# Optimization experiments

Measured on AMD Instinct MI355X. Metric: run time of the kernel, lower is better.

## Reference

```python
import jax, jax.numpy as jnp
import numpy as np

EMBED_DIM = 1024
NUM_HEADS = 16
HEAD_DIM = EMBED_DIM // NUM_HEADS


def setup_inputs() -> dict:
    key = jax.random.key(0)
    k_x, k_qw, k_qb, k_ow, k_ob = jax.random.split(key, 5)
    B, T, C = 2, 2048, EMBED_DIM
    scale = 1.0 / np.sqrt(C)
    return {
        "x": jax.random.normal(k_x, (B, T, C), dtype=jnp.float32),
        "qkv_w": jax.random.normal(k_qw, (C, 3 * C), dtype=jnp.float32) * scale,
        "qkv_b": jax.random.normal(k_qb, (3 * C,), dtype=jnp.float32) * 0.02,
        "out_w": jax.random.normal(k_ow, (C, C), dtype=jnp.float32) * scale,
        "out_b": jax.random.normal(k_ob, (C,), dtype=jnp.float32) * 0.02,
    }


def reference(x, qkv_w, qkv_b, out_w, out_b):
    # x: (B, T, C). Causal masked multi-head self-attention (eval mode: dropout off).
    B, T, C = x.shape
    H, Dh = NUM_HEADS, HEAD_DIM
    qkv = x @ qkv_w + qkv_b                      # (B, T, 3C)
    qkv = qkv.reshape(B, T, 3, H, Dh)
    q = jnp.transpose(qkv[:, :, 0], (0, 2, 1, 3))  # (B, H, T, Dh)
    k = jnp.transpose(qkv[:, :, 1], (0, 2, 1, 3))
    v = jnp.transpose(qkv[:, :, 2], (0, 2, 1, 3))
    scores = jnp.einsum("bhqd,bhkd->bhqk", q, k) / np.sqrt(Dh)
    causal = jnp.tril(jnp.ones((T, T), dtype=bool))
    scores = jnp.where(causal[None, None], scores, -jnp.inf)
    attn = jax.nn.softmax(scores, axis=-1)        # (B, H, T, T)
    out = jnp.einsum("bhqk,bhkd->bhqd", attn, v)  # (B, H, T, Dh)
    out = jnp.transpose(out, (0, 2, 1, 3)).reshape(B, T, C)
    return out @ out_w + out_b
```

## Files before the change

### kernel.cpp

```cpp
#include <hip/hip_runtime.h>


typedef __bf16 bf16;
typedef __attribute__((ext_vector_type(4))) __bf16 bf16x4;
typedef __attribute__((ext_vector_type(8))) __bf16 bf16x8;
typedef __attribute__((ext_vector_type(4))) float f32x4;

#define T_SEQ 2048
#define NHEAD 16
#define QSCALE 0.1803368801111244f

__device__ __forceinline__ void async16(const bf16* g, const bf16* l) {
    __builtin_amdgcn_global_load_lds(
        (const __attribute__((address_space(1))) void*)g,
        (__attribute__((address_space(3))) void*)l, 16, 0, 0);
}


__global__ void cvt_f32_bf16(const float* __restrict__ in, bf16* __restrict__ out, int n) {
    int i = (blockIdx.x * blockDim.x + threadIdx.x) * 4;
    if (i < n) {
        float4 v = *(const float4*)(in + i);
        bf16x4 o;
        o.x = (bf16)v.x; o.y = (bf16)v.y; o.z = (bf16)v.z; o.w = (bf16)v.w;
        *(bf16x4*)(out + i) = o;
    }
}

__global__ void transpose_cvt(const float* __restrict__ in, bf16* __restrict__ out,
                              int K_, int N_) {
    __shared__ float tile[32][33];
    int k0 = blockIdx.x * 32, n0 = blockIdx.y * 32;
    int tx = threadIdx.x, ty = threadIdx.y;
    for (int r = 0; r < 32; r += 8)
        tile[ty + r][tx] = in[(k0 + ty + r) * N_ + n0 + tx];
    __syncthreads();
    for (int r = 0; r < 32; r += 8)
        out[(n0 + ty + r) * K_ + k0 + tx] = (bf16)tile[tx][ty + r];
}


__global__ __launch_bounds__(256) void gemm_qkv(
    const bf16* __restrict__ A, const bf16* __restrict__ Bt,
    const float* __restrict__ bias,
    bf16* __restrict__ Qo, bf16* __restrict__ Ko, bf16* __restrict__ Vt) {
    __shared__ __align__(16) bf16 As[128 * 32];
    __shared__ __align__(16) bf16 Bs[128 * 32];
    const int t = threadIdx.x;
    const int lane = t & 63, wave = t >> 6;
    const int l15 = lane & 15, quad = lane >> 4;
    const int wm = wave & 1, wn = wave >> 1;
    const int m0 = blockIdx.y * 128, n0 = blockIdx.x * 128;

    f32x4 acc[4][4] = {};

    const bf16* ag = A + (m0 + (t >> 2)) * 1024 + (t & 3) * 8;
    const bf16* bg = Bt + (n0 + (t >> 2)) * 1024 + (t & 3) * 8;
    bf16* as0 = As + wave * 512;
    bf16* as1 = As + 2048 + wave * 512;
    bf16* bs0 = Bs + wave * 512;
    bf16* bs1 = Bs + 2048 + wave * 512;

    for (int k0 = 0; k0 < 1024; k0 += 32) {
        async16(ag + k0, as0);
        async16(ag + 64 * 1024 + k0, as1);
        async16(bg + k0, bs0);
        async16(bg + 64 * 1024 + k0, bs1);
        __syncthreads();
        bf16x8 af[4], bfr[4];
        for (int i = 0; i < 4; i++)
            af[i] = *(const bf16x8*)(As + (wm * 64 + i * 16 + l15) * 32 + quad * 8);
        for (int j = 0; j < 4; j++)
            bfr[j] = *(const bf16x8*)(Bs + (wn * 64 + j * 16 + l15) * 32 + quad * 8);
        for (int i = 0; i < 4; i++)
            for (int j = 0; j < 4; j++)
                acc[i][j] = __builtin_amdgcn_mfma_f32_16x16x32_bf16(af[i], bfr[j], acc[i][j], 0, 0, 0);
        __syncthreads();
    }

    for (int i = 0; i < 4; i++) {
        for (int j = 0; j < 4; j++) {
            int col = n0 + wn * 64 + j * 16 + l15;
            float bv = bias[col];
            int sec = col >> 10, c2 = col & 1023, h = c2 >> 6, d = c2 & 63;
            for (int r = 0; r < 4; r++) {
                int row = m0 + wm * 64 + i * 16 + quad * 4 + r;
                int b = row >> 11, tt = row & 2047;
                int bh = b * NHEAD + h;
                float v = acc[i][j][r] + bv;
                if (sec == 0)
                    Qo[(bh * T_SEQ + tt) * 64 + d] = (bf16)(v * QSCALE);
                else if (sec == 1)
                    Ko[(bh * T_SEQ + tt) * 64 + d] = (bf16)v;
                else
                    Vt[(bh * 64 + d) * T_SEQ + tt] = (bf16)v;
            }
        }
    }
}

#define PSTR 64
__global__ __launch_bounds__(256, 4) void attn(
    const bf16* __restrict__ Q, const bf16* __restrict__ K,
    const bf16* __restrict__ Vt, bf16* __restrict__ AO) {
    __shared__ __align__(16) bf16 Ks[2][64 * 64];
    __shared__ __align__(16) bf16 Vs[2][64 * 64];
    __shared__ __align__(16) bf16 Pb[4][16 * PSTR];
    const int lane = threadIdx.x & 63, wave = threadIdx.x >> 6;
    const int l15 = lane & 15, quad = lane >> 4;
    const int lin = blockIdx.x;
    const int s = lin >> 3;
    const int bh = ((lin & 7) << 2) | (s & 3);
    const int k5 = s >> 2;
    const int R = (k5 & 1) ? (k5 >> 1) : (31 - (k5 >> 1));
    const int Rb = R * 64;

    const bf16* qp = Q + (bh * T_SEQ + Rb + wave * 16) * 64;
    const bf16* kp = K + bh * T_SEQ * 64;
    const bf16* vp = Vt + bh * 64 * T_SEQ;
    bf16* pw = &Pb[wave][0];

    bf16x8 qf0 = *(const bf16x8*)(qp + l15 * 64 + quad * 8);
    bf16x8 qf1 = *(const bf16x8*)(qp + l15 * 64 + 32 + quad * 8);

    f32x4 acc[4] = {};
    float lsum[4] = {0.f, 0.f, 0.f, 0.f};

    const int sx = (quad ^ (l15 & 7)) << 3;

    auto stage = [&](int kb, int b) {
        const bf16* kg = kp + kb * 64;
        for (int i = 0; i < 2; i++) {
            int G = (wave * 2 + i) * 64 + lane;
            int key = G >> 3, p = G & 7;
            async16(kg + key * 64 + ((p ^ (key & 7)) << 3), &Ks[b][(wave * 2 + i) * 512]);
        }
        for (int i = 0; i < 2; i++) {
            int d = (wave * 2 + i) * 8 + (lane >> 3);
            async16(vp + d * T_SEQ + kb + (((lane & 7) ^ (d & 7)) << 3),
                    &Vs[b][(wave * 2 + i) * 512]);
        }
    };

    stage(0, 0);
    for (int c = 0; c <= R; c++) {
        __syncthreads();
        if (c < R) stage((c + 1) * 64, (c + 1) & 1);
        const bf16* ksb = &Ks[c & 1][0];
        const bf16* vsb = &Vs[c & 1][0];
        const bool dg = (c == R);
        const int na = dg ? (wave + 1) : 4;
        const int kb = c * 64;

        f32x4 sc[4];
        for (int n = 0; n < 4; n++) {
            if (n < na) {
                const bf16* kbase = ksb + (n * 16 + l15) * 64;
                bf16x8 kf0 = *(const bf16x8*)(kbase + sx);
                bf16x8 kf1 = *(const bf16x8*)(kbase + (sx ^ 32));
                f32x4 z = {};
                z = __builtin_amdgcn_mfma_f32_16x16x32_bf16(qf0, kf0, z, 0, 0, 0);
                z = __builtin_amdgcn_mfma_f32_16x16x32_bf16(qf1, kf1, z, 0, 0, 0);
                sc[n] = z;
            }
        }
        for (int n = 0; n < 4; n++) {
            for (int r = 0; r < 4; r++) {
                float e = 0.0f;
                if (n < na) {
                    float v = sc[n][r];
                    if (dg && n == na - 1) {
                        int key = kb + n * 16 + l15;
                        int qrow = Rb + wave * 16 + quad * 4 + r;
                        if (key > qrow) v = -100000.0f;
                    }
                    e = __builtin_amdgcn_exp2f(v);
                }
                lsum[r] += e;
                pw[(quad * 4 + r) * PSTR + n * 16 + l15] = (bf16)e;
            }
        }
        __builtin_amdgcn_s_waitcnt(0xC07F);
        bf16x8 pf0 = *(const bf16x8*)(pw + l15 * PSTR + quad * 8);
        bf16x8 pf1 = *(const bf16x8*)(pw + l15 * PSTR + 32 + quad * 8);
        for (int j = 0; j < 4; j++) {
            const bf16* vbase = vsb + (j * 16 + l15) * 64;
            bf16x8 vf0 = *(const bf16x8*)(vbase + sx);
            bf16x8 vf1 = *(const bf16x8*)(vbase + (sx ^ 32));
            acc[j] = __builtin_amdgcn_mfma_f32_16x16x32_bf16(pf0, vf0, acc[j], 0, 0, 0);
            acc[j] = __builtin_amdgcn_mfma_f32_16x16x32_bf16(pf1, vf1, acc[j], 0, 0, 0);
        }
    }

    float linv[4];
    for (int r = 0; r < 4; r++) {
        float v = lsum[r];
        v += __shfl_xor(v, 1, 16);
        v += __shfl_xor(v, 2, 16);
        v += __shfl_xor(v, 4, 16);
        v += __shfl_xor(v, 8, 16);
        linv[r] = 1.0f / v;
    }
    const int b = bh >> 4, h = bh & 15;
    bf16* aop = AO + (b * T_SEQ + Rb + wave * 16) * 1024 + h * 64;
    for (int r = 0; r < 4; r++)
        for (int j = 0; j < 4; j++)
            aop[(quad * 4 + r) * 1024 + j * 16 + l15] = (bf16)(acc[j][r] * linv[r]);
}

__global__ __launch_bounds__(256) void gemm_out_k(
    const bf16* __restrict__ A, const bf16* __restrict__ Bt,
    const float* __restrict__ bias, float* __restrict__ out) {
    __shared__ __align__(16) bf16 As[128 * 32];
    __shared__ __align__(16) bf16 Bs[128 * 32];
    const int t = threadIdx.x;
    const int lane = t & 63, wave = t >> 6;
    const int l15 = lane & 15, quad = lane >> 4;
    const int wm = wave & 1, wn = wave >> 1;
    const int m0 = blockIdx.y * 128, n0 = blockIdx.x * 128;

    f32x4 acc[4][4] = {};

    const bf16* ag = A + (m0 + (t >> 2)) * 1024 + (t & 3) * 8;
    const bf16* bg = Bt + (n0 + (t >> 2)) * 1024 + (t & 3) * 8;
    bf16* as0 = As + wave * 512;
    bf16* as1 = As + 2048 + wave * 512;
    bf16* bs0 = Bs + wave * 512;
    bf16* bs1 = Bs + 2048 + wave * 512;

    for (int k0 = 0; k0 < 1024; k0 += 32) {
        async16(ag + k0, as0);
        async16(ag + 64 * 1024 + k0, as1);
        async16(bg + k0, bs0);
        async16(bg + 64 * 1024 + k0, bs1);
        __syncthreads();
        bf16x8 af[4], bfr[4];
        for (int i = 0; i < 4; i++)
            af[i] = *(const bf16x8*)(As + (wm * 64 + i * 16 + l15) * 32 + quad * 8);
        for (int j = 0; j < 4; j++)
            bfr[j] = *(const bf16x8*)(Bs + (wn * 64 + j * 16 + l15) * 32 + quad * 8);
        for (int i = 0; i < 4; i++)
            for (int j = 0; j < 4; j++)
                acc[i][j] = __builtin_amdgcn_mfma_f32_16x16x32_bf16(af[i], bfr[j], acc[i][j], 0, 0, 0);
        __syncthreads();
    }

    for (int i = 0; i < 4; i++) {
        for (int j = 0; j < 4; j++) {
            int col = n0 + wn * 64 + j * 16 + l15;
            float bv = bias[col];
            for (int r = 0; r < 4; r++) {
                int row = m0 + wm * 64 + i * 16 + quad * 4 + r;
                out[row * 1024 + col] = acc[i][j][r] + bv;
            }
        }
    }
}

extern "C" void kernel_launch(void* const* d_in, const int* in_sizes, int n_in,
                              void* d_out, int out_size, void* d_ws, size_t ws_size,
                              hipStream_t stream) {
    const float* x     = (const float*)d_in[0];
    const float* qkv_w = (const float*)d_in[1];
    const float* qkv_b = (const float*)d_in[2];
    const float* out_w = (const float*)d_in[3];
    const float* out_b = (const float*)d_in[4];
    float* out = (float*)d_out;

    char* ws = (char*)d_ws;
    bf16* xb   = (bf16*)(ws);
    bf16* wbT  = (bf16*)(ws + (8ull << 20));
    bf16* owbT = (bf16*)(ws + (14ull << 20));
    bf16* Qb   = (bf16*)(ws + (16ull << 20));
    bf16* Kb   = (bf16*)(ws + (24ull << 20));
    bf16* Vt   = (bf16*)(ws + (32ull << 20));
    bf16* AO   = (bf16*)(ws + (40ull << 20));

    cvt_f32_bf16<<<4096, 256, 0, stream>>>(x, xb, 2 * 2048 * 1024);
    transpose_cvt<<<dim3(32, 96), dim3(32, 8), 0, stream>>>(qkv_w, wbT, 1024, 3072);
    transpose_cvt<<<dim3(32, 32), dim3(32, 8), 0, stream>>>(out_w, owbT, 1024, 1024);
    gemm_qkv<<<dim3(24, 32), 256, 0, stream>>>(xb, wbT, qkv_b, Qb, Kb, Vt);
    attn<<<1024, 256, 0, stream>>>(Qb, Kb, Vt, AO);
    gemm_out_k<<<dim3(8, 32), 256, 0, stream>>>(AO, owbT, out_b, out);
}
```

Baseline: 203.4 us.

## Merge prep kernels and restructure attention into 128-row paired causal tiles

```diff
diff --git a/kernel.cpp b/kernel.cpp
--- a/kernel.cpp
+++ b/kernel.cpp
@@ -16,22 +16,27 @@
         (__attribute__((address_space(3))) void*)l, 16, 0, 0);
 }
 
-
-__global__ void cvt_f32_bf16(const float* __restrict__ in, bf16* __restrict__ out, int n) {
-    int i = (blockIdx.x * blockDim.x + threadIdx.x) * 4;
-    if (i < n) {
-        float4 v = *(const float4*)(in + i);
+__global__ __launch_bounds__(256) void prep(
+    const float* __restrict__ x, bf16* __restrict__ xb,
+    const float* __restrict__ qkv_w, bf16* __restrict__ wbT,
+    const float* __restrict__ out_w, bf16* __restrict__ owbT) {
+    const int bid = blockIdx.x, tid = threadIdx.x;
+    if (bid < 4096) {
+        int i = (bid * 256 + tid) * 4;
+        float4 v = *(const float4*)(x + i);
         bf16x4 o;
         o.x = (bf16)v.x; o.y = (bf16)v.y; o.z = (bf16)v.z; o.w = (bf16)v.w;
-        *(bf16x4*)(out + i) = o;
-    }
-}
-
-__global__ void transpose_cvt(const float* __restrict__ in, bf16* __restrict__ out,
-                              int K_, int N_) {
+        *(bf16x4*)(xb + i) = o;
+        return;
+    }
     __shared__ float tile[32][33];
-    int k0 = blockIdx.x * 32, n0 = blockIdx.y * 32;
-    int tx = threadIdx.x, ty = threadIdx.y;
+    const float* in;
+    bf16* out;
+    int K_, N_, b;
+    if (bid < 7168) { b = bid - 4096; in = qkv_w; out = wbT; K_ = 1024; N_ = 3072; }
+    else            { b = bid - 7168; in = out_w; out = owbT; K_ = 1024; N_ = 1024; }
+    int k0 = (b & 31) * 32, n0 = (b >> 5) * 32;
+    int tx = tid & 31, ty = tid >> 5;
     for (int r = 0; r < 32; r += 8)
         tile[ty + r][tx] = in[(k0 + ty + r) * N_ + n0 + tx];
     __syncthreads();
@@ -100,112 +105,111 @@
 }
 
 #define PSTR 64
-__global__ __launch_bounds__(256, 4) void attn(
+__global__ __launch_bounds__(512, 2) void attn(
     const bf16* __restrict__ Q, const bf16* __restrict__ K,
     const bf16* __restrict__ Vt, bf16* __restrict__ AO) {
     __shared__ __align__(16) bf16 Ks[2][64 * 64];
     __shared__ __align__(16) bf16 Vs[2][64 * 64];
-    __shared__ __align__(16) bf16 Pb[4][16 * PSTR];
-    const int lane = threadIdx.x & 63, wave = threadIdx.x >> 6;
+    __shared__ __align__(16) bf16 Pb[8][16 * PSTR];
+    const int tid = threadIdx.x;
+    const int lane = tid & 63, wave = tid >> 6;
     const int l15 = lane & 15, quad = lane >> 4;
-    const int lin = blockIdx.x;
-    const int s = lin >> 3;
-    const int bh = ((lin & 7) << 2) | (s & 3);
-    const int k5 = s >> 2;
-    const int R = (k5 & 1) ? (k5 >> 1) : (31 - (k5 >> 1));
-    const int Rb = R * 64;
-
-    const bf16* qp = Q + (bh * T_SEQ + Rb + wave * 16) * 64;
+    const int bh = ((blockIdx.x & 7) << 2) | ((blockIdx.x >> 3) & 3);
+    const int pr = blockIdx.x >> 5;
+
     const bf16* kp = K + bh * T_SEQ * 64;
     const bf16* vp = Vt + bh * 64 * T_SEQ;
     bf16* pw = &Pb[wave][0];
-
-    bf16x8 qf0 = *(const bf16x8*)(qp + l15 * 64 + quad * 8);
-    bf16x8 qf1 = *(const bf16x8*)(qp + l15 * 64 + 32 + quad * 8);
-
-    f32x4 acc[4] = {};
-    float lsum[4] = {0.f, 0.f, 0.f, 0.f};
+    const int b_ = bh >> 4, h_ = bh & 15;
 
     const int sx = (quad ^ (l15 & 7)) << 3;
 
     auto stage = [&](int kb, int b) {
-        const bf16* kg = kp + kb * 64;
-        for (int i = 0; i < 2; i++) {
-            int G = (wave * 2 + i) * 64 + lane;
-            int key = G >> 3, p = G & 7;
-            async16(kg + key * 64 + ((p ^ (key & 7)) << 3), &Ks[b][(wave * 2 + i) * 512]);
-        }
-        for (int i = 0; i < 2; i++) {
-            int d = (wave * 2 + i) * 8 + (lane >> 3);
-            async16(vp + d * T_SEQ + kb + (((lane & 7) ^ (d & 7)) << 3),
-                    &Vs[b][(wave * 2 + i) * 512]);
-        }
+        int rowi = tid >> 3, p = tid & 7;
+        const bf16* ksrc = kp + (kb + rowi) * 64 + ((p ^ (rowi & 7)) << 3);
+        async16(ksrc, &Ks[b][wave * 512]);
+        const bf16* vsrc = vp + rowi * T_SEQ + kb + ((p ^ (rowi & 7)) << 3);
+        async16(vsrc, &Vs[b][wave * 512]);
     };
 
-    stage(0, 0);
-    for (int c = 0; c <= R; c++) {
-        __syncthreads();
-        if (c < R) stage((c + 1) * 64, (c + 1) & 1);
-        const bf16* ksb = &Ks[c & 1][0];
-        const bf16* vsb = &Vs[c & 1][0];
-        const bool dg = (c == R);
-        const int na = dg ? (wave + 1) : 4;
-        const int kb = c * 64;
-
-        f32x4 sc[4];
-        for (int n = 0; n < 4; n++) {
-            if (n < na) {
-                const bf16* kbase = ksb + (n * 16 + l15) * 64;
-                bf16x8 kf0 = *(const bf16x8*)(kbase + sx);
-                bf16x8 kf1 = *(const bf16x8*)(kbase + (sx ^ 32));
-                f32x4 z = {};
-                z = __builtin_amdgcn_mfma_f32_16x16x32_bf16(qf0, kf0, z, 0, 0, 0);
-                z = __builtin_amdgcn_mfma_f32_16x16x32_bf16(qf1, kf1, z, 0, 0, 0);
-                sc[n] = z;
+    for (int half = 0; half < 2; half++) {
+        const int qt = half ? pr : (15 - pr);
+        const int t0 = qt * 128 + wave * 16;
+        const int m = t0 >> 4;
+        const bf16* qp = Q + (bh * T_SEQ + t0) * 64;
+        bf16x8 qf0 = *(const bf16x8*)(qp + l15 * 64 + quad * 8);
+        bf16x8 qf1 = *(const bf16x8*)(qp + l15 * 64 + 32 + quad * 8);
+
+        f32x4 acc[4] = {};
+        float lsum[4] = {0.f, 0.f, 0.f, 0.f};
+
+        const int C = 2 * qt + 2;
+        stage(0, 0);
+        for (int c = 0; c < C; c++) {
+            __syncthreads();
+            if (c + 1 < C) stage((c + 1) * 64, (c + 1) & 1);
+            const int nr = m - 4 * c + 1;
+            if (nr > 0) {
+                const int na = min(4, nr);
+                const bool dg = (nr <= 4);
+                const bf16* ksb = &Ks[c & 1][0];
+                const bf16* vsb = &Vs[c & 1][0];
+
+                f32x4 sc[4];
+                for (int n = 0; n < 4; n++) {
+                    if (n < na) {
+                        const bf16* kbase = ksb + (n * 16 + l15) * 64;
+                        bf16x8 kf0 = *(const bf16x8*)(kbase + sx);
+                        bf16x8 kf1 = *(const bf16x8*)(kbase + (sx ^ 32));
+                        f32x4 z = {};
+                        z = __builtin_amdgcn_mfma_f32_16x16x32_bf16(qf0, kf0, z, 0, 0, 0);
+                        z = __builtin_amdgcn_mfma_f32_16x16x32_bf16(qf1, kf1, z, 0, 0, 0);
+                        sc[n] = z;
+                    }
+                }
+                for (int n = 0; n < 4; n++) {
+                    for (int r = 0; r < 4; r++) {
+                        float e = 0.0f;
+                        if (n < na) {
+                            float v = sc[n][r];
+                            if (dg && n == na - 1) {
+                                int key = c * 64 + n * 16 + l15;
+                                int qrow = t0 + quad * 4 + r;
+                                if (key > qrow) v = -100000.0f;
+                            }
+                            e = __builtin_amdgcn_exp2f(v);
+                        }
+                        lsum[r] += e;
+                        pw[(quad * 4 + r) * PSTR + n * 16 + l15] = (bf16)e;
+                    }
+                }
+                __builtin_amdgcn_s_waitcnt(0xC07F);
+                bf16x8 pf0 = *(const bf16x8*)(pw + l15 * PSTR + quad * 8);
+                bf16x8 pf1 = *(const bf16x8*)(pw + l15 * PSTR + 32 + quad * 8);
+                for (int j = 0; j < 4; j++) {
+                    const bf16* vbase = vsb + (j * 16 + l15) * 64;
+                    bf16x8 vf0 = *(const bf16x8*)(vbase + sx);
+                    bf16x8 vf1 = *(const bf16x8*)(vbase + (sx ^ 32));
+                    acc[j] = __builtin_amdgcn_mfma_f32_16x16x32_bf16(pf0, vf0, acc[j], 0, 0, 0);
+                    acc[j] = __builtin_amdgcn_mfma_f32_16x16x32_bf16(pf1, vf1, acc[j], 0, 0, 0);
+                }
             }
         }
-        for (int n = 0; n < 4; n++) {
-            for (int r = 0; r < 4; r++) {
-                float e = 0.0f;
-                if (n < na) {
-                    float v = sc[n][r];
-                    if (dg && n == na - 1) {
-                        int key = kb + n * 16 + l15;
-                        int qrow = Rb + wave * 16 + quad * 4 + r;
-                        if (key > qrow) v = -100000.0f;
-                    }
-                    e = __builtin_amdgcn_exp2f(v);
-                }
-                lsum[r] += e;
-                pw[(quad * 4 + r) * PSTR + n * 16 + l15] = (bf16)e;
-            }
-        }
-        __builtin_amdgcn_s_waitcnt(0xC07F);
-        bf16x8 pf0 = *(const bf16x8*)(pw + l15 * PSTR + quad * 8);
-        bf16x8 pf1 = *(const bf16x8*)(pw + l15 * PSTR + 32 + quad * 8);
-        for (int j = 0; j < 4; j++) {
-            const bf16* vbase = vsb + (j * 16 + l15) * 64;
-            bf16x8 vf0 = *(const bf16x8*)(vbase + sx);
-            bf16x8 vf1 = *(const bf16x8*)(vbase + (sx ^ 32));
-            acc[j] = __builtin_amdgcn_mfma_f32_16x16x32_bf16(pf0, vf0, acc[j], 0, 0, 0);
-            acc[j] = __builtin_amdgcn_mfma_f32_16x16x32_bf16(pf1, vf1, acc[j], 0, 0, 0);
-        }
-    }
-
-    float linv[4];
-    for (int r = 0; r < 4; r++) {
-        float v = lsum[r];
-        v += __shfl_xor(v, 1, 16);
-        v += __shfl_xor(v, 2, 16);
-        v += __shfl_xor(v, 4, 16);
-        v += __shfl_xor(v, 8, 16);
-        linv[r] = 1.0f / v;
-    }
-    const int b = bh >> 4, h = bh & 15;
-    bf16* aop = AO + (b * T_SEQ + Rb + wave * 16) * 1024 + h * 64;
-    for (int r = 0; r < 4; r++)
-        for (int j = 0; j < 4; j++)
-            aop[(quad * 4 + r) * 1024 + j * 16 + l15] = (bf16)(acc[j][r] * linv[r]);
+
+        float linv[4];
+        for (int r = 0; r < 4; r++) {
+            float v = lsum[r];
+            v += __shfl_xor(v, 1, 16);
+            v += __shfl_xor(v, 2, 16);
+            v += __shfl_xor(v, 4, 16);
+            v += __shfl_xor(v, 8, 16);
+            linv[r] = 1.0f / v;
+        }
+        bf16* aop = AO + (b_ * T_SEQ + t0) * 1024 + h_ * 64;
+        for (int r = 0; r < 4; r++)
+            for (int j = 0; j < 4; j++)
+                aop[(quad * 4 + r) * 1024 + j * 16 + l15] = (bf16)(acc[j][r] * linv[r]);
+    }
 }
 
 __global__ __launch_bounds__(256) void gemm_out_k(
@@ -276,10 +280,8 @@
     bf16* Vt   = (bf16*)(ws + (32ull << 20));
     bf16* AO   = (bf16*)(ws + (40ull << 20));
 
-    cvt_f32_bf16<<<4096, 256, 0, stream>>>(x, xb, 2 * 2048 * 1024);
-    transpose_cvt<<<dim3(32, 96), dim3(32, 8), 0, stream>>>(qkv_w, wbT, 1024, 3072);
-    transpose_cvt<<<dim3(32, 32), dim3(32, 8), 0, stream>>>(out_w, owbT, 1024, 1024);
+    prep<<<8192, 256, 0, stream>>>(x, xb, qkv_w, wbT, out_w, owbT);
     gemm_qkv<<<dim3(24, 32), 256, 0, stream>>>(xb, wbT, qkv_b, Qb, Kb, Vt);
-    attn<<<1024, 256, 0, stream>>>(Qb, Kb, Vt, AO);
+    attn<<<256, 512, 0, stream>>>(Qb, Kb, Vt, AO);
     gemm_out_k<<<dim3(8, 32), 256, 0, stream>>>(AO, owbT, out_b, out);
 }
```

After: 202.4 us. Within noise of the previous version (-0.5%).
